# Kernel optimization log

Measured on AMD Instinct MI355X. Metric: run time of the kernel, lower is better.

The kernel has to match this reference:

```python
import jax, jax.numpy as jnp
import numpy as np

DMIN, DMAX = -1.0, 1.0
B, I, O, K = 1024, 256, 256, 128

def setup_inputs() -> dict:
    key = jax.random.key(0)
    k1, k2, k3 = jax.random.split(key, 3)
    x = jax.random.normal(k1, (B, I), dtype=jnp.float32)
    bound = 1.0 / np.sqrt(I)
    base_weight = jax.random.uniform(k2, (O, I), dtype=jnp.float32, minval=-bound, maxval=bound)
    coeff = 0.03 * jax.random.normal(k3, (O, I, K), dtype=jnp.float32)
    coeff = coeff - coeff.mean(axis=-1, keepdims=True)
    return {
        'x': x,
        'base_weight': base_weight,
        'spline_coefficients': coeff,
        'spline_scale': jnp.ones((O, I), dtype=jnp.float32),
        'bias': jnp.zeros((O,), dtype=jnp.float32),
    }


def reference(x, base_weight, spline_coefficients, spline_scale, bias):
    num_knots = spline_coefficients.shape[-1]
    step = (DMAX - DMIN) / (num_knots - 1)
    # input activation (tanh) then clamp to spline domain
    p = jnp.tanh(x)                                   # (B, I)
    c = jnp.clip(p, DMIN, DMAX)
    scaled = (c - DMIN) / step                        # in [0, K-1]
    left = jnp.clip(jnp.floor(scaled).astype(jnp.int32), 0, num_knots - 1)
    right = jnp.minimum(left + 1, num_knots - 1)
    frac = scaled - left.astype(p.dtype)              # (B, I)
    # fold spline_scale into coefficients, then gather only the 2 relevant knots
    Cs = spline_coefficients * spline_scale[..., None]  # (O, I, K)
    ii = jnp.arange(x.shape[1])[None, :]                # (1, I) broadcasts with (B, I)
    cl = Cs[:, ii, left]                                # (O, B, I)
    cr = Cs[:, ii, right]                               # (O, B, I)
    spline = jnp.einsum('bi,obi->bo', 1.0 - frac, cl) + jnp.einsum('bi,obi->bo', frac, cr)
    base = jax.nn.silu(p) @ base_weight.T               # (B, O)
    return base + spline + bias[None, :]
```

## Files before the change

kernel.cpp:

```cpp
#include <hip/hip_runtime.h>

constexpr int Bb = 1024;
constexpr int Ii = 256;
constexpr int Oo = 256;
constexpr int Kk = 128;

typedef unsigned short u16;
typedef u16 ushort4v __attribute__((ext_vector_type(4)));

__device__ __forceinline__ float bf16u_to_f(u16 u) {
    union { unsigned int ui; float f; } c;
    c.ui = ((unsigned int)u) << 16;
    return c.f;
}
__device__ __forceinline__ u16 f_to_bf16(float f) {
    union { float f; unsigned int u; } c; c.f = f;
    unsigned int r = c.u + 0x7fffu + ((c.u >> 16) & 1u);
    return (u16)(r >> 16);
}

__global__ void kprep(const float* __restrict__ x, const float* __restrict__ wbase,
                      const float* __restrict__ bias, float4* __restrict__ fls,
                      float* __restrict__ wt, float* __restrict__ out) {
    int tid = blockIdx.x * 256 + threadIdx.x;
    float xv = x[tid];
    float e2 = __expf(2.f * xv);
    float p = 1.f - 2.f / (e2 + 1.f);
    float s = p / (1.f + __expf(-p));
    float c = fminf(fmaxf(p, -1.f), 1.f);
    float scaled = (c + 1.f) * ((float)(Kk - 1) * 0.5f);
    int l = (int)floorf(scaled);
    l = min(max(l, 0), Kk - 1);
    int r = min(l + 1, Kk - 1);
    float f = scaled - (float)l;
    float4 v;
    v.x = f;
    v.y = s;
    v.z = __int_as_float(l * (Oo * 2));
    v.w = __int_as_float(r * (Oo * 2));
    fls[tid] = v;

    out[tid] = bias[tid & (Oo - 1)];
    if (tid < Ii * Oo) wt[tid] = wbase[(tid & 255) * Ii + (tid >> 8)];
}

__global__ __launch_bounds__(256) void kperm(const float* __restrict__ cs,
                                             const float* __restrict__ scale,
                                             u16* __restrict__ cp) {
    __shared__ u16 T[128 * 130];
    int i  = blockIdx.x >> 1;
    int o0 = (blockIdx.x & 1) << 7;
    int t = threadIdx.x;

    {
        int c4 = t & 31;
        int rb = t >> 5;
        const float4* cs4 = (const float4*)cs;
#pragma unroll
        for (int p = 0; p < 16; ++p) {
            int r = p * 8 + rb;
            int o = o0 + r;
            float sc = scale[o * Ii + i];
            float4 val = cs4[(size_t)(o * Ii + i) * (Kk / 4) + c4];
            unsigned int lo = ((unsigned int)f_to_bf16(val.y * sc) << 16) | f_to_bf16(val.x * sc);
            unsigned int hi = ((unsigned int)f_to_bf16(val.w * sc) << 16) | f_to_bf16(val.z * sc);
            *(unsigned int*)&T[r * 130 + c4 * 4]     = lo;
            *(unsigned int*)&T[r * 130 + c4 * 4 + 2] = hi;
        }
    }
    __syncthreads();
    {
        int ol = t & 127;
        int kh = t >> 7;
        u16* dst = cp + ((size_t)i * Kk) * Oo + o0 + ol;
#pragma unroll
        for (int p = 0; p < 64; ++p) {
            int k = p * 2 + kh;
            dst[(size_t)k * Oo] = T[ol * 130 + k];
        }
    }
}

__global__ __launch_bounds__(256, 4) void kmain(const float4* __restrict__ fls,
                                                const char* __restrict__ cpb,
                                                const float4* __restrict__ wt4,
                                                float* __restrict__ out) {
    __shared__ float4 sf[128];
    int t = threadIdx.x;
    int blk = blockIdx.x;
    int chunk = blk & 7;
    int b0 = (blk >> 3) << 2;
    int i0 = chunk << 5;

    if (t < 128) {
        int il = t >> 2, bl = t & 3;
        sf[t] = fls[(size_t)(b0 + bl) * Ii + i0 + il];
    }
    __syncthreads();

    int oq = t & 63;
    int bh = t >> 6;

    float a0 = 0.f, a1 = 0.f, a2 = 0.f, a3 = 0.f;
    const char* cbase = cpb + (size_t)i0 * (Kk * Oo * 2) + oq * 8;
#pragma unroll 4
    for (int il = 0; il < 32; ++il) {
        float4 v = sf[il * 4 + bh];
        float4 w = wt4[(i0 + il) * (Oo / 4) + oq];
        const char* ci = cbase + (size_t)il * (Kk * Oo * 2);
        ushort4v cl = *(const ushort4v*)(ci + __float_as_int(v.z));
        ushort4v cr = *(const ushort4v*)(ci + __float_as_int(v.w));
        float f = v.x, g = 1.f - v.x, s = v.y;
        a0 = fmaf(s, w.x, a0);
        a1 = fmaf(s, w.y, a1);
        a2 = fmaf(s, w.z, a2);
        a3 = fmaf(s, w.w, a3);
        a0 = fmaf(g, bf16u_to_f(cl.x), a0);
        a1 = fmaf(g, bf16u_to_f(cl.y), a1);
        a2 = fmaf(g, bf16u_to_f(cl.z), a2);
        a3 = fmaf(g, bf16u_to_f(cl.w), a3);
        a0 = fmaf(f, bf16u_to_f(cr.x), a0);
        a1 = fmaf(f, bf16u_to_f(cr.y), a1);
        a2 = fmaf(f, bf16u_to_f(cr.z), a2);
        a3 = fmaf(f, bf16u_to_f(cr.w), a3);
    }
    float* op = out + (size_t)(b0 + bh) * Oo + oq * 4;
    atomicAdd(op + 0, a0);
    atomicAdd(op + 1, a1);
    atomicAdd(op + 2, a2);
    atomicAdd(op + 3, a3);
}

extern "C" void kernel_launch(void* const* d_in, const int* in_sizes, int n_in,
                              void* d_out, int out_size, void* d_ws, size_t ws_size,
                              hipStream_t stream) {
    const float* x     = (const float*)d_in[0];
    const float* wbase = (const float*)d_in[1];
    const float* coeff = (const float*)d_in[2];
    const float* scale = (const float*)d_in[3];
    const float* bias  = (const float*)d_in[4];
    float* out = (float*)d_out;

    char* ws = (char*)d_ws;
    float4* fls = (float4*)ws;
    size_t off = (size_t)Bb * Ii * sizeof(float4);
    u16* cp = (u16*)(ws + off);
    off += (size_t)Ii * Kk * Oo * sizeof(u16);
    float* wt = (float*)(ws + off);

    kprep<<<(Bb * Ii) / 256, 256, 0, stream>>>(x, wbase, bias, fls, wt, out);
    kperm<<<Ii * 2, 256, 0, stream>>>(coeff, scale, cp);
    kmain<<<2048, 256, 0, stream>>>(fls, (const char*)cp, (const float4*)wt, out);
}
```

Before: 127.4 us.

## Replace atomic output accumulation with per-chunk partials and a reduce kernel

The main kernel now writes each input-chunk's partial sums as float4 to a workspace buffer instead of issuing four float atomicAdds per thread into the output. A new reduce kernel sums the 8 partials, adds the bias, and writes the output, which removes the bias init from the prep kernel. The inner loop unroll also goes from 4 to 8. This avoids atomic contention but adds an extra launch and about 8 MB of partial-buffer traffic.

```diff
diff --git a/kernel.cpp b/kernel.cpp
--- a/kernel.cpp
+++ b/kernel.cpp
@@ -4,6 +4,7 @@
 constexpr int Ii = 256;
 constexpr int Oo = 256;
 constexpr int Kk = 128;
+constexpr int NCH = 8;
 
 typedef unsigned short u16;
 typedef u16 ushort4v __attribute__((ext_vector_type(4)));
@@ -20,8 +21,7 @@
 }
 
 __global__ void kprep(const float* __restrict__ x, const float* __restrict__ wbase,
-                      const float* __restrict__ bias, float4* __restrict__ fls,
-                      float* __restrict__ wt, float* __restrict__ out) {
+                      float4* __restrict__ fls, float* __restrict__ wt) {
     int tid = blockIdx.x * 256 + threadIdx.x;
     float xv = x[tid];
     float e2 = __expf(2.f * xv);
@@ -40,7 +40,6 @@
     v.w = __int_as_float(r * (Oo * 2));
     fls[tid] = v;
 
-    out[tid] = bias[tid & (Oo - 1)];
     if (tid < Ii * Oo) wt[tid] = wbase[(tid & 255) * Ii + (tid >> 8)];
 }
 
@@ -84,11 +83,11 @@
 __global__ __launch_bounds__(256, 4) void kmain(const float4* __restrict__ fls,
                                                 const char* __restrict__ cpb,
                                                 const float4* __restrict__ wt4,
-                                                float* __restrict__ out) {
+                                                float4* __restrict__ part4) {
     __shared__ float4 sf[128];
     int t = threadIdx.x;
     int blk = blockIdx.x;
-    int chunk = blk & 7;
+    int chunk = blk & (NCH - 1);
     int b0 = (blk >> 3) << 2;
     int i0 = chunk << 5;
 
@@ -103,7 +102,7 @@
 
     float a0 = 0.f, a1 = 0.f, a2 = 0.f, a3 = 0.f;
     const char* cbase = cpb + (size_t)i0 * (Kk * Oo * 2) + oq * 8;
-#pragma unroll 4
+#pragma unroll 8
     for (int il = 0; il < 32; ++il) {
         float4 v = sf[il * 4 + bh];
         float4 w = wt4[(i0 + il) * (Oo / 4) + oq];
@@ -124,11 +123,24 @@
         a2 = fmaf(f, bf16u_to_f(cr.z), a2);
         a3 = fmaf(f, bf16u_to_f(cr.w), a3);
     }
-    float* op = out + (size_t)(b0 + bh) * Oo + oq * 4;
-    atomicAdd(op + 0, a0);
-    atomicAdd(op + 1, a1);
-    atomicAdd(op + 2, a2);
-    atomicAdd(op + 3, a3);
+    float4 r; r.x = a0; r.y = a1; r.z = a2; r.w = a3;
+    part4[(size_t)chunk * (Bb * Oo / 4) + (size_t)(b0 + bh) * (Oo / 4) + oq] = r;
+}
+
+__global__ __launch_bounds__(256) void kreduce(const float4* __restrict__ part4,
+                                               const float4* __restrict__ bias4,
+                                               float4* __restrict__ out4) {
+    int gid = blockIdx.x * 256 + threadIdx.x;
+    const float4* p = part4 + gid;
+    float4 s = p[0];
+#pragma unroll
+    for (int c = 1; c < NCH; ++c) {
+        float4 v = p[(size_t)c * (Bb * Oo / 4)];
+        s.x += v.x; s.y += v.y; s.z += v.z; s.w += v.w;
+    }
+    float4 bv = bias4[gid & 63];
+    s.x += bv.x; s.y += bv.y; s.z += bv.z; s.w += bv.w;
+    out4[gid] = s;
 }
 
 extern "C" void kernel_launch(void* const* d_in, const int* in_sizes, int n_in,
@@ -147,8 +159,11 @@
     u16* cp = (u16*)(ws + off);
     off += (size_t)Ii * Kk * Oo * sizeof(u16);
     float* wt = (float*)(ws + off);
+    off += (size_t)Ii * Oo * sizeof(float);
+    float4* part4 = (float4*)(ws + off);
 
-    kprep<<<(Bb * Ii) / 256, 256, 0, stream>>>(x, wbase, bias, fls, wt, out);
+    kprep<<<(Bb * Ii) / 256, 256, 0, stream>>>(x, wbase, fls, wt);
     kperm<<<Ii * 2, 256, 0, stream>>>(coeff, scale, cp);
-    kmain<<<2048, 256, 0, stream>>>(fls, (const char*)cp, (const float4*)wt, out);
+    kmain<<<2048, 256, 0, stream>>>(fls, (const char*)cp, (const float4*)wt, part4);
+    kreduce<<<(Bb * Oo / 4) / 256, 256, 0, stream>>>(part4, (const float4*)bias, (float4*)out);
 }
```

Result: faster. 116.8 us (-8.4%).
